# Kernel tuning notes

Hardware: AMD Instinct MI355X
Metric: run time of the kernel (lower is better)

Reference implementation:

```python
import jax, jax.numpy as jnp
import numpy as np

N_NODES = 50000
IN_CH, HID_CH, OUT_CH = 128, 128, 16
N_EDGES = 800000


def setup_inputs() -> dict:
    key = jax.random.key(0)
    ks = jax.random.split(key, 10)
    def lin_w(k, fan_in, fan_out):
        bound = 1.0 / np.sqrt(fan_in)
        return jax.random.uniform(k, (fan_in, fan_out), jnp.float32, -bound, bound)
    inp = {
        'x': jax.random.normal(ks[0], (N_NODES, IN_CH), jnp.float32),
        'edge_index': jax.random.randint(ks[1], (2, N_EDGES), 0, N_NODES, jnp.int64),
        # SAGEConv l/r weights: lin_l (neighbor aggregate, with bias), lin_r (root, no bias)
        'W1_l': lin_w(ks[2], IN_CH, HID_CH), 'b1': jnp.zeros((HID_CH,), jnp.float32),
        'W1_r': lin_w(ks[3], IN_CH, HID_CH),
        'W2_l': lin_w(ks[4], HID_CH, HID_CH), 'b2': jnp.zeros((HID_CH,), jnp.float32),
        'W2_r': lin_w(ks[5], HID_CH, HID_CH),
        'W3_l': lin_w(ks[6], HID_CH, HID_CH), 'b3': jnp.zeros((HID_CH,), jnp.float32),
        'W3_r': lin_w(ks[7], HID_CH, HID_CH),
        'W_lin': lin_w(ks[8], HID_CH, OUT_CH), 'b_lin': jnp.zeros((OUT_CH,), jnp.float32),
    }
    return inp


def _sage_conv(x, src, dst, W_l, b_l, W_r, n_nodes):
    # mean aggregation of source-node features at destination nodes
    msg_sum = jax.ops.segment_sum(x[src], dst, num_segments=n_nodes)  # [N, d]
    deg = jax.ops.segment_sum(jnp.ones((src.shape[0],), x.dtype), dst, num_segments=n_nodes)
    mean = msg_sum / jnp.maximum(deg, 1.0)[:, None]
    return mean @ W_l + b_l + x @ W_r


def reference(x, edge_index, W1_l, b1, W1_r, W2_l, b2, W2_r, W3_l, b3, W3_r, W_lin, b_lin):
    src, dst = edge_index[0], edge_index[1]
    n = x.shape[0]
    h = jax.nn.relu(_sage_conv(x, src, dst, W1_l, b1, W1_r, n))
    h = jax.nn.relu(_sage_conv(h, src, dst, W2_l, b2, W2_r, n))
    # dropout is identity in eval mode
    h = jax.nn.relu(_sage_conv(h, src, dst, W3_l, b3, W3_r, n))
    return h @ W_lin + b_lin
```

## Files before the change

### kernel.cpp

```cpp
#include <hip/hip_runtime.h>


typedef short bf16x8 __attribute__((ext_vector_type(8)));
typedef float f32x4 __attribute__((ext_vector_type(4)));

__device__ __forceinline__ float bf16_to_f32(unsigned int lo16) {
  unsigned int u = lo16 << 16;
  return __builtin_bit_cast(float, u);
}
__device__ __forceinline__ unsigned short f32_to_bf16(float f) {
  unsigned int u = __builtin_bit_cast(unsigned int, f);
  unsigned int r = (u + 0x7FFFu + ((u >> 16) & 1u)) >> 16;
  return (unsigned short)r;
}

__device__ __forceinline__ void gload_lds16(void* g, void* lds_base) {
  __builtin_amdgcn_global_load_lds(
      (__attribute__((address_space(1))) unsigned int*)(uintptr_t)g,
      (__attribute__((address_space(3))) unsigned int*)(unsigned int)(uintptr_t)lds_base,
      16, 0, 0);
}

__global__ void k_zero_i32(int* __restrict__ p, int n) {
  int i = blockIdx.x * blockDim.x + threadIdx.x;
  if (i < n) p[i] = 0;
}

__global__ __launch_bounds__(256) void k_split(const float* __restrict__ in,
                                               unsigned short* __restrict__ hi,
                                               unsigned short* __restrict__ lo, int n4) {
  int i = blockIdx.x * blockDim.x + threadIdx.x;
  if (i < n4) {
    float4 v = *reinterpret_cast<const float4*>(&in[(size_t)i * 4]);
    ushort4 h, l;
    h.x = f32_to_bf16(v.x); l.x = f32_to_bf16(v.x - bf16_to_f32(h.x));
    h.y = f32_to_bf16(v.y); l.y = f32_to_bf16(v.y - bf16_to_f32(h.y));
    h.z = f32_to_bf16(v.z); l.z = f32_to_bf16(v.z - bf16_to_f32(h.z));
    h.w = f32_to_bf16(v.w); l.w = f32_to_bf16(v.w - bf16_to_f32(h.w));
    *reinterpret_cast<ushort4*>(&hi[(size_t)i * 4]) = h;
    *reinterpret_cast<ushort4*>(&lo[(size_t)i * 4]) = l;
  }
}

__global__ __launch_bounds__(256) void k_prep_w(const float* __restrict__ Wl,
                                                const float* __restrict__ Wr,
                                                unsigned short* __restrict__ Whi,
                                                unsigned short* __restrict__ Wlo) {
  int n = blockIdx.x, k = threadIdx.x;
  float v = (k < 128) ? Wl[(size_t)k * 128 + n] : Wr[(size_t)(k - 128) * 128 + n];
  unsigned short h = f32_to_bf16(v);
  Whi[(size_t)n * 256 + k] = h;
  Wlo[(size_t)n * 256 + k] = f32_to_bf16(v - bf16_to_f32(h));
}

__global__ void k_detect(const int* __restrict__ ei, int* __restrict__ flag) {
  int t = threadIdx.x;
  int any = 0;
  for (int i = t; i < 1024; i += 256)
    if (ei[2 * i + 1] != 0) any = 1;
  if (any) atomicOr(flag, 1);
}

__device__ __forceinline__ int load_src(const int* ei, int E, int i, int is32) {
  return is32 ? ei[i] : ei[2 * i];
}
__device__ __forceinline__ int load_dst(const int* ei, int E, int i, int is32) {
  return is32 ? ei[E + i] : ei[2 * E + 2 * i];
}

__global__ __launch_bounds__(256) void k_count(const int* __restrict__ ei,
                                               const int* __restrict__ flag,
                                               int* __restrict__ deg,
                                               int* __restrict__ erank, int E) {
  int i = blockIdx.x * blockDim.x + threadIdx.x;
  if (i < E) {
    int is32 = *flag;
    erank[i] = atomicAdd(&deg[load_dst(ei, E, i, is32)], 1);
  }
}

__global__ __launch_bounds__(256) void k_scan1(const int* __restrict__ deg,
                                               int* __restrict__ bsum, int N) {
  __shared__ int s[256];
  int t = threadIdx.x;
  int base = blockIdx.x * 1024 + t * 4;
  int v = 0;
#pragma unroll
  for (int j = 0; j < 4; ++j) {
    int i = base + j;
    v += (i < N) ? deg[i] : 0;
  }
  s[t] = v;
  __syncthreads();
  for (int off = 128; off > 0; off >>= 1) {
    if (t < off) s[t] += s[t + off];
    __syncthreads();
  }
  if (t == 0) bsum[blockIdx.x] = s[0];
}

__global__ __launch_bounds__(1024) void k_scan2(int* __restrict__ bsum,
                                                int* __restrict__ row_ptr,
                                                int nb, int N) {
  __shared__ int s[1024];
  int t = threadIdx.x;
  int v = (t < nb) ? bsum[t] : 0;
  s[t] = v;
  __syncthreads();
  for (int off = 1; off < 1024; off <<= 1) {
    int add = (t >= off) ? s[t - off] : 0;
    __syncthreads();
    s[t] += add;
    __syncthreads();
  }
  if (t < nb) bsum[t] = s[t] - v;
  if (t == 1023) row_ptr[N] = s[1023];
}

__global__ __launch_bounds__(256) void k_scan3(const int* __restrict__ deg,
                                               const int* __restrict__ bsum,
                                               int* __restrict__ row_ptr,
                                               float* __restrict__ inv_deg, int N) {
  __shared__ int s[256];
  int t = threadIdx.x;
  int base = blockIdx.x * 1024 + t * 4;
  int v[4];
  int sum = 0;
#pragma unroll
  for (int j = 0; j < 4; ++j) {
    int i = base + j;
    v[j] = (i < N) ? deg[i] : 0;
    sum += v[j];
  }
  s[t] = sum;
  __syncthreads();
  for (int off = 1; off < 256; off <<= 1) {
    int add = (t >= off) ? s[t - off] : 0;
    __syncthreads();
    s[t] += add;
    __syncthreads();
  }
  int excl = s[t] - sum + bsum[blockIdx.x];
#pragma unroll
  for (int j = 0; j < 4; ++j) {
    int i = base + j;
    if (i < N) {
      row_ptr[i] = excl;
      inv_deg[i] = 1.0f / (float)((v[j] > 1) ? v[j] : 1);
      excl += v[j];
    }
  }
}

__global__ __launch_bounds__(256) void k_fill(const int* __restrict__ ei,
                                              const int* __restrict__ flag,
                                              const int* __restrict__ row_ptr,
                                              const int* __restrict__ erank,
                                              int* __restrict__ col_idx, int E) {
  int i = blockIdx.x * blockDim.x + threadIdx.x;
  if (i < E) {
    int is32 = *flag;
    int d = load_dst(ei, E, i, is32);
    int s = load_src(ei, E, i, is32);
    col_idx[row_ptr[d] + erank[i]] = s;
  }
}

__global__ __launch_bounds__(256) void k_aggregate(const unsigned short* __restrict__ Xhi,
                                                   const int* __restrict__ row_ptr,
                                                   const int* __restrict__ col_idx,
                                                   const float* __restrict__ inv_deg,
                                                   unsigned int* __restrict__ Mhi,
                                                   unsigned int* __restrict__ Mlo, int N) {
  int gw = (int)((blockIdx.x * blockDim.x + threadIdx.x) >> 6);
  int lane = threadIdx.x & 63;
  if (gw >= N) return;
  int s = row_ptr[gw], e = row_ptr[gw + 1];
  float ax0 = 0.f, ay0 = 0.f, ax1 = 0.f, ay1 = 0.f;
  float ax2 = 0.f, ay2 = 0.f, ax3 = 0.f, ay3 = 0.f;
  int j = s;
  for (; j + 4 <= e; j += 4) {
    int c0 = col_idx[j], c1 = col_idx[j + 1], c2 = col_idx[j + 2], c3 = col_idx[j + 3];
    unsigned int v0 = *reinterpret_cast<const unsigned int*>(&Xhi[(size_t)c0 * 128 + lane * 2]);
    unsigned int v1 = *reinterpret_cast<const unsigned int*>(&Xhi[(size_t)c1 * 128 + lane * 2]);
    unsigned int v2 = *reinterpret_cast<const unsigned int*>(&Xhi[(size_t)c2 * 128 + lane * 2]);
    unsigned int v3 = *reinterpret_cast<const unsigned int*>(&Xhi[(size_t)c3 * 128 + lane * 2]);
    ax0 += bf16_to_f32(v0 & 0xFFFFu); ay0 += bf16_to_f32(v0 >> 16);
    ax1 += bf16_to_f32(v1 & 0xFFFFu); ay1 += bf16_to_f32(v1 >> 16);
    ax2 += bf16_to_f32(v2 & 0xFFFFu); ay2 += bf16_to_f32(v2 >> 16);
    ax3 += bf16_to_f32(v3 & 0xFFFFu); ay3 += bf16_to_f32(v3 >> 16);
  }
  for (; j < e; ++j) {
    int c = col_idx[j];
    unsigned int v = *reinterpret_cast<const unsigned int*>(&Xhi[(size_t)c * 128 + lane * 2]);
    ax0 += bf16_to_f32(v & 0xFFFFu); ay0 += bf16_to_f32(v >> 16);
  }
  float inv = inv_deg[gw];
  float rx = (ax0 + ax1 + ax2 + ax3) * inv;
  float ry = (ay0 + ay1 + ay2 + ay3) * inv;
  unsigned int hx = f32_to_bf16(rx), hy = f32_to_bf16(ry);
  unsigned int lx = f32_to_bf16(rx - bf16_to_f32(hx));
  unsigned int ly = f32_to_bf16(ry - bf16_to_f32(hy));
  Mhi[(size_t)gw * 64 + lane] = hx | (hy << 16);
  Mlo[(size_t)gw * 64 + lane] = lx | (ly << 16);
}

__global__ __launch_bounds__(256) void k_mfma_gemm(
    const unsigned short* __restrict__ A1hi, const unsigned short* __restrict__ A1lo,
    const unsigned short* __restrict__ A2hi, const unsigned short* __restrict__ A2lo,
    const unsigned short* __restrict__ Whi, const unsigned short* __restrict__ Wlo,
    const float* __restrict__ bias,
    unsigned short* __restrict__ Ohi, unsigned short* __restrict__ Olo, int N) {
  __shared__ unsigned short sAhi[128 * 32], sAlo[128 * 32];
  __shared__ unsigned short sBhi[128 * 32], sBlo[128 * 32];
  int t = threadIdx.x;
  int lane = t & 63;
  int w = t >> 6;
  int wr = (w >> 1) * 64, wc = (w & 1) * 64;
  int block_row = blockIdx.x * 128;

  f32x4 acc[4][4];
#pragma unroll
  for (int m = 0; m < 4; ++m)
#pragma unroll
    for (int n = 0; n < 4; ++n) acc[m][n] = f32x4{0.f, 0.f, 0.f, 0.f};

  int kg = lane & 3;
  int rr = lane >> 2;
  int fr = lane & 15;
  int fkb = (lane >> 4) * 16;

  for (int kt = 0; kt < 8; ++kt) {
    {
      const unsigned short* gsrc;
      unsigned short* lbase;
      int isA = (w < 2);
      if (w == 0) { gsrc = (kt < 4) ? A1hi : A2hi; lbase = sAhi; }
      else if (w == 1) { gsrc = (kt < 4) ? A1lo : A2lo; lbase = sAlo; }
      else if (w == 2) { gsrc = Whi; lbase = sBhi; }
      else { gsrc = Wlo; lbase = sBlo; }
#pragma unroll
      for (int c = 0; c < 8; ++c) {
        int idx = c * 16 + rr;
        const char* src;
        if (isA) {
          int rg = block_row + idx;
          if (rg > N - 1) rg = N - 1;
          src = (const char*)gsrc + (size_t)rg * 256 + (kt & 3) * 64 + kg * 16;
        } else {
          src = (const char*)gsrc + (size_t)idx * 512 + kt * 64 + kg * 16;
        }
        gload_lds16((void*)src, (char*)lbase + c * 1024);
      }
    }
    __syncthreads();
    bf16x8 a_hi[4], a_lo[4], b_hi[4], b_lo[4];
#pragma unroll
    for (int m = 0; m < 4; ++m) {
      int row = wr + m * 16 + fr;
      a_hi[m] = *reinterpret_cast<const bf16x8*>((const char*)sAhi + row * 64 + fkb);
      a_lo[m] = *reinterpret_cast<const bf16x8*>((const char*)sAlo + row * 64 + fkb);
    }
#pragma unroll
    for (int n = 0; n < 4; ++n) {
      int col = wc + n * 16 + fr;
      b_hi[n] = *reinterpret_cast<const bf16x8*>((const char*)sBhi + col * 64 + fkb);
      b_lo[n] = *reinterpret_cast<const bf16x8*>((const char*)sBlo + col * 64 + fkb);
    }
#pragma unroll
    for (int m = 0; m < 4; ++m)
#pragma unroll
      for (int n = 0; n < 4; ++n) {
        acc[m][n] = __builtin_amdgcn_mfma_f32_16x16x32_bf16(a_hi[m], b_hi[n], acc[m][n], 0, 0, 0);
        acc[m][n] = __builtin_amdgcn_mfma_f32_16x16x32_bf16(a_hi[m], b_lo[n], acc[m][n], 0, 0, 0);
        acc[m][n] = __builtin_amdgcn_mfma_f32_16x16x32_bf16(a_lo[m], b_hi[n], acc[m][n], 0, 0, 0);
      }
    __syncthreads();
  }

  float bv[4];
#pragma unroll
  for (int n = 0; n < 4; ++n) bv[n] = bias[wc + n * 16 + (lane & 15)];
#pragma unroll
  for (int m = 0; m < 4; ++m) {
#pragma unroll
    for (int n = 0; n < 4; ++n) {
#pragma unroll
      for (int j = 0; j < 4; ++j) {
        int row_l = wr + m * 16 + (lane >> 4) * 4 + j;
        int g = block_row + row_l;
        if (g < N) {
          int col = wc + n * 16 + (lane & 15);
          float v = fmaxf(acc[m][n][j] + bv[n], 0.f);
          unsigned short h = f32_to_bf16(v);
          Ohi[(size_t)g * 128 + col] = h;
          Olo[(size_t)g * 128 + col] = f32_to_bf16(v - bf16_to_f32(h));
        }
      }
    }
  }
}

__global__ __launch_bounds__(256) void k_final(const unsigned short* __restrict__ Hhi,
                                               const unsigned short* __restrict__ Hlo,
                                               const float* __restrict__ W,
                                               const float* __restrict__ b,
                                               float* __restrict__ Out, int N) {
  __shared__ float sH[16][128];
  __shared__ float sW[128][16];
  __shared__ float sb[16];
  int t = threadIdx.x;
  int node0 = blockIdx.x * 16;
  {
    int row = t >> 4, q = t & 15;
    int g = node0 + row;
    if (g < N) {
      uint4 hv = *reinterpret_cast<const uint4*>(&Hhi[(size_t)g * 128 + q * 8]);
      uint4 lv = *reinterpret_cast<const uint4*>(&Hlo[(size_t)g * 128 + q * 8]);
      const unsigned short* hp = (const unsigned short*)&hv;
      const unsigned short* lp = (const unsigned short*)&lv;
#pragma unroll
      for (int e = 0; e < 8; ++e)
        sH[row][q * 8 + e] = bf16_to_f32(hp[e]) + bf16_to_f32(lp[e]);
    } else {
#pragma unroll
      for (int e = 0; e < 8; ++e) sH[row][q * 8 + e] = 0.f;
    }
  }
  for (int j = t; j < 512; j += 256) {
    int row = j >> 2, q = j & 3;
    *reinterpret_cast<float4*>(&sW[row][q * 4]) =
        *reinterpret_cast<const float4*>(&W[(size_t)row * 16 + q * 4]);
  }
  if (t < 16) sb[t] = b[t];
  __syncthreads();
  int node = t >> 4, col = t & 15;
  float acc = sb[col];
#pragma unroll 8
  for (int k = 0; k < 128; ++k) acc = fmaf(sH[node][k], sW[k][col], acc);
  int g = node0 + node;
  if (g < N) Out[(size_t)g * 16 + col] = acc;
}

extern "C" void kernel_launch(void* const* d_in, const int* in_sizes, int n_in,
                              void* d_out, int out_size, void* d_ws, size_t ws_size,
                              hipStream_t stream) {
  if (n_in < 13) return;
  const float* x = (const float*)d_in[0];
  const int* ei = (const int*)d_in[1];
  const float* W1l = (const float*)d_in[2];
  const float* b1 = (const float*)d_in[3];
  const float* W1r = (const float*)d_in[4];
  const float* W2l = (const float*)d_in[5];
  const float* b2 = (const float*)d_in[6];
  const float* W2r = (const float*)d_in[7];
  const float* W3l = (const float*)d_in[8];
  const float* b3 = (const float*)d_in[9];
  const float* W3r = (const float*)d_in[10];
  const float* Wlin = (const float*)d_in[11];
  const float* blin = (const float*)d_in[12];
  float* out = (float*)d_out;

  const int N = in_sizes[0] / 128;
  const int E = in_sizes[1] / 2;

  char* w = (char*)d_ws;
  size_t off = 0;
  auto alloc = [&](size_t bytes) -> void* {
    off = (off + 255) & ~(size_t)255;
    void* p = (void*)(w + off);
    off += bytes;
    return p;
  };
  size_t actB = (size_t)N * 128 * 2;
  unsigned short* Xhi = (unsigned short*)alloc(actB);
  unsigned short* Xlo = (unsigned short*)alloc(actB);
  unsigned short* Ahi = (unsigned short*)alloc(actB);
  unsigned short* Alo = (unsigned short*)alloc(actB);
  unsigned short* Mhi = (unsigned short*)alloc(actB);
  unsigned short* Mlo = (unsigned short*)alloc(actB);
  unsigned short* Wt[6];
  for (int i = 0; i < 6; ++i) Wt[i] = (unsigned short*)alloc(128 * 256 * 2);
  int* deg = (int*)alloc((size_t)N * 4);
  int* row_ptr = (int*)alloc((size_t)(N + 1) * 4);
  int* col_idx = (int*)alloc((size_t)E * 4);
  int* erank = (int*)alloc((size_t)E * 4);
  float* invdeg = (float*)alloc((size_t)N * 4);
  int* flag = (int*)alloc(4);
  int* bsum = (int*)alloc((size_t)1024 * 4);
  (void)ws_size;

  const int nbScan = (N + 1023) / 1024;

  k_zero_i32<<<(N + 255) / 256, 256, 0, stream>>>(deg, N);
  k_zero_i32<<<1, 256, 0, stream>>>(flag, 1);
  k_detect<<<1, 256, 0, stream>>>(ei, flag);
  k_count<<<(E + 255) / 256, 256, 0, stream>>>(ei, flag, deg, erank, E);
  k_split<<<(N * 32 + 255) / 256, 256, 0, stream>>>(x, Xhi, Xlo, N * 32);
  k_prep_w<<<128, 256, 0, stream>>>(W1l, W1r, Wt[0], Wt[1]);
  k_prep_w<<<128, 256, 0, stream>>>(W2l, W2r, Wt[2], Wt[3]);
  k_prep_w<<<128, 256, 0, stream>>>(W3l, W3r, Wt[4], Wt[5]);
  k_scan1<<<nbScan, 256, 0, stream>>>(deg, bsum, N);
  k_scan2<<<1, 1024, 0, stream>>>(bsum, row_ptr, nbScan, N);
  k_scan3<<<nbScan, 256, 0, stream>>>(deg, bsum, row_ptr, invdeg, N);
  k_fill<<<(E + 255) / 256, 256, 0, stream>>>(ei, flag, row_ptr, erank, col_idx, E);

  int aggBlocks = (N * 64 + 255) / 256;
  int gemmBlocks = (N + 127) / 128;

  k_aggregate<<<aggBlocks, 256, 0, stream>>>(Xhi, row_ptr, col_idx, invdeg,
                                             (unsigned int*)Mhi, (unsigned int*)Mlo, N);
  k_mfma_gemm<<<gemmBlocks, 256, 0, stream>>>(Mhi, Mlo, Xhi, Xlo, Wt[0], Wt[1], b1,
                                              Ahi, Alo, N);
  k_aggregate<<<aggBlocks, 256, 0, stream>>>(Ahi, row_ptr, col_idx, invdeg,
                                             (unsigned int*)Mhi, (unsigned int*)Mlo, N);
  k_mfma_gemm<<<gemmBlocks, 256, 0, stream>>>(Mhi, Mlo, Ahi, Alo, Wt[2], Wt[3], b2,
                                              Xhi, Xlo, N);
  k_aggregate<<<aggBlocks, 256, 0, stream>>>(Xhi, row_ptr, col_idx, invdeg,
                                             (unsigned int*)Mhi, (unsigned int*)Mlo, N);
  k_mfma_gemm<<<gemmBlocks, 256, 0, stream>>>(Mhi, Mlo, Xhi, Xlo, Wt[4], Wt[5], b3,
                                              Ahi, Alo, N);
  k_final<<<(N + 15) / 16, 256, 0, stream>>>(Ahi, Alo, Wlin, blin, out, N);
}
```

Baseline: 290.8 us.

## Split neighbor aggregation into four feature-slice passes with edge-parallel lanes

Replaces the single aggregation kernel for the first two layers with four launches, each gathering a 32-column slice of features. Within a wave, four lane groups handle different edges, and partial sums are combined with cross-lane shuffles. The goal is a gathered working set per pass that fits better in cache, plus more edges in flight per node. The cost is four launches per layer, re-reading row_ptr and col_idx four times, and 64-byte gather segments instead of 256-byte rows.

```diff
diff --git a/kernel.cpp b/kernel.cpp
--- a/kernel.cpp
+++ b/kernel.cpp
@@ -203,6 +203,53 @@
   unsigned int ly = f32_to_bf16(ry - bf16_to_f32(hy));
   Mhi[(size_t)gw * 64 + lane] = hx | (hy << 16);
   Mlo[(size_t)gw * 64 + lane] = lx | (ly << 16);
+}
+
+__global__ __launch_bounds__(256) void k_agg_slice(const unsigned short* __restrict__ Xhi,
+                                                   const int* __restrict__ row_ptr,
+                                                   const int* __restrict__ col_idx,
+                                                   const float* __restrict__ inv_deg,
+                                                   unsigned int* __restrict__ Mhi,
+                                                   unsigned int* __restrict__ Mlo,
+                                                   int N, int slice) {
+  int gw = (int)((blockIdx.x * blockDim.x + threadIdx.x) >> 6);
+  int lane = threadIdx.x & 63;
+  if (gw >= N) return;
+  int g = lane >> 4;
+  int sl = lane & 15;
+  int s = row_ptr[gw], e = row_ptr[gw + 1];
+  const unsigned short* base = Xhi + slice * 32 + sl * 2;
+  float a0 = 0.f, a1 = 0.f, b0 = 0.f, b1 = 0.f;
+  int j = s + g;
+  for (; j + 4 < e; j += 8) {
+    int c0 = col_idx[j];
+    int c1 = col_idx[j + 4];
+    unsigned int v0 = *reinterpret_cast<const unsigned int*>(base + (size_t)c0 * 128);
+    unsigned int v1 = *reinterpret_cast<const unsigned int*>(base + (size_t)c1 * 128);
+    a0 += bf16_to_f32(v0 & 0xFFFFu); a1 += bf16_to_f32(v0 >> 16);
+    b0 += bf16_to_f32(v1 & 0xFFFFu); b1 += bf16_to_f32(v1 >> 16);
+  }
+  if (j < e) {
+    int c0 = col_idx[j];
+    unsigned int v0 = *reinterpret_cast<const unsigned int*>(base + (size_t)c0 * 128);
+    a0 += bf16_to_f32(v0 & 0xFFFFu); a1 += bf16_to_f32(v0 >> 16);
+  }
+  float r0 = a0 + b0, r1 = a1 + b1;
+  r0 += __shfl_xor(r0, 16, 64);
+  r0 += __shfl_xor(r0, 32, 64);
+  r1 += __shfl_xor(r1, 16, 64);
+  r1 += __shfl_xor(r1, 32, 64);
+  float inv = inv_deg[gw];
+  r0 *= inv;
+  r1 *= inv;
+  unsigned int h0 = f32_to_bf16(r0), h1 = f32_to_bf16(r1);
+  if (g == 0) {
+    Mhi[(size_t)gw * 64 + slice * 16 + sl] = h0 | (h1 << 16);
+  } else if (g == 1) {
+    unsigned int l0 = f32_to_bf16(r0 - bf16_to_f32(h0));
+    unsigned int l1 = f32_to_bf16(r1 - bf16_to_f32(h1));
+    Mlo[(size_t)gw * 64 + slice * 16 + sl] = l0 | (l1 << 16);
+  }
 }
 
 __global__ __launch_bounds__(256) void k_mfma_gemm(
@@ -408,12 +455,16 @@
   int aggBlocks = (N * 64 + 255) / 256;
   int gemmBlocks = (N + 127) / 128;
 
-  k_aggregate<<<aggBlocks, 256, 0, stream>>>(Xhi, row_ptr, col_idx, invdeg,
-                                             (unsigned int*)Mhi, (unsigned int*)Mlo, N);
+  for (int s = 0; s < 4; ++s)
+    k_agg_slice<<<aggBlocks, 256, 0, stream>>>(Xhi, row_ptr, col_idx, invdeg,
+                                               (unsigned int*)Mhi, (unsigned int*)Mlo,
+                                               N, s);
   k_mfma_gemm<<<gemmBlocks, 256, 0, stream>>>(Mhi, Mlo, Xhi, Xlo, Wt[0], Wt[1], b1,
                                               Ahi, Alo, N);
-  k_aggregate<<<aggBlocks, 256, 0, stream>>>(Ahi, row_ptr, col_idx, invdeg,
-                                             (unsigned int*)Mhi, (unsigned int*)Mlo, N);
+  for (int s = 0; s < 4; ++s)
+    k_agg_slice<<<aggBlocks, 256, 0, stream>>>(Ahi, row_ptr, col_idx, invdeg,
+                                               (unsigned int*)Mhi, (unsigned int*)Mlo,
+                                               N, s);
   k_mfma_gemm<<<gemmBlocks, 256, 0, stream>>>(Mhi, Mlo, Ahi, Alo, Wt[2], Wt[3], b2,
                                               Xhi, Xlo, N);
   k_aggregate<<<aggBlocks, 256, 0, stream>>>(Xhi, row_ptr, col_idx, invdeg,
```

After: 401.0 us. 1.38x slower.
